# Kernel tuning notes

Measured on AMD Instinct MI355X. Metric: run time of the kernel, lower is better.

Reference implementation:

```python
import jax, jax.numpy as jnp
import numpy as np


def reference(x, edge_index, edge_attr, W, b):
    """PyG GCNConv: out = D^{-1/2} (A + I) D^{-1/2} X W + b.

    x: [N, Din] node features
    edge_index: [2, E] int (row=source, col=target)
    edge_attr: [E] edge weights
    W: [Din, Dout], b: [Dout]
    """
    N = x.shape[0]
    # add self-loops with weight 1 (PyG fill_value=1.0)
    loop = jnp.arange(N, dtype=edge_index.dtype)
    row = jnp.concatenate([edge_index[0], loop])
    col = jnp.concatenate([edge_index[1], loop])
    w = jnp.concatenate([edge_attr, jnp.ones((N,), dtype=edge_attr.dtype)])

    # symmetric normalization: norm_e = d[row]^-1/2 * w_e * d[col]^-1/2
    deg = jax.ops.segment_sum(w, col, num_segments=N)
    dis = jnp.where(deg > 0, jax.lax.rsqrt(jnp.where(deg > 0, deg, 1.0)), 0.0)
    norm = dis[row] * w * dis[col]

    # linear projection first (Din == Dout, cheaper either way), then
    # gather-scale-scatter aggregation at targets
    h = x @ W                                   # [N, Dout]
    msg = h[row] * norm[:, None]                # [E+N, Dout]
    out = jax.ops.segment_sum(msg, col, num_segments=N)  # [N, Dout]
    return out + b


def setup_inputs() -> dict:
    key = jax.random.key(0)
    k1, k2, k3, k4 = jax.random.split(key, 4)
    N, E, Din, Dout = 100000, 1600000, 128, 128
    x = jax.random.normal(k1, (N, Din), dtype=jnp.float32)
    edge_index = jax.random.randint(k2, (2, E), 0, N, dtype=jnp.int64)
    edge_attr = jax.random.uniform(k3, (E,), dtype=jnp.float32)
    # Glorot init like PyG Linear default
    W = jax.random.normal(k4, (Din, Dout), dtype=jnp.float32) * (1.0 / np.sqrt(Din))
    b = jnp.zeros((Dout,), dtype=jnp.float32)
    return {"x": x, "edge_index": edge_index, "edge_attr": edge_attr, "W": W, "b": b}
```

## Files before the change

### kernel.cpp

```cpp
#include <hip/hip_runtime.h>


#define ELEMS_PER_SCAN_BLOCK 4096
#define SCAN_SHIFT 12
#define CHUNK 2048
#define NCMAX 800

typedef __attribute__((ext_vector_type(8))) short short8;
typedef __attribute__((ext_vector_type(4))) float f32x4;

__device__ inline unsigned short f2bf(float f) {
    unsigned u = __float_as_uint(f);
    u += 0x7fffu + ((u >> 16) & 1u);
    return (unsigned short)(u >> 16);
}
__device__ inline float bf_lo(unsigned u) { return __uint_as_float(u << 16); }
__device__ inline float bf_hi(unsigned u) { return __uint_as_float(u & 0xffff0000u); }

__global__ __launch_bounds__(256) void k_hist(const int* __restrict__ col,
                                              const float* __restrict__ W,
                                              int* __restrict__ histg,
                                              unsigned short* __restrict__ Wtg,
                                              int E, int NC, int NBLK) {
    __shared__ int lh[1024];
    int t = threadIdx.x, blk = blockIdx.x;
    if (blk < 64) {
        int n = blk * 2 + (t >> 7);
        int k = t & 127;
        Wtg[n * 128 + k] = f2bf(W[k * 128 + n]);
    }
    for (int i = t; i < 1024; i += 256) lh[i] = 0;
    __syncthreads();
    int base = blk * CHUNK;
    #pragma unroll
    for (int i = 0; i < CHUNK / 256; ++i) {
        int e = base + i * 256 + t;
        if (e < E) atomicAdd(&lh[col[e] >> 7], 1);
    }
    __syncthreads();
    for (int b = t; b < NC; b += 256) histg[b * NBLK + blk] = lh[b];
}

__device__ inline int wave_incl_scan(int x, int lane) {
    #pragma unroll
    for (int d = 1; d < 64; d <<= 1) {
        int y = __shfl_up(x, d, 64);
        if (lane >= d) x += y;
    }
    return x;
}

__global__ void k_scan1(const int* __restrict__ in, int* __restrict__ out,
                        int* __restrict__ bsum, int M) {
    __shared__ int wsum[4];
    __shared__ int woff[4];
    int t = threadIdx.x, lane = t & 63, wid = t >> 6;
    int base = blockIdx.x * ELEMS_PER_SCAN_BLOCK + t * 16;
    int v[16];
    #pragma unroll
    for (int i = 0; i < 16; ++i) v[i] = (base + i < M) ? in[base + i] : 0;
    int run = 0;
    #pragma unroll
    for (int i = 0; i < 16; ++i) { int x = v[i]; v[i] = run; run += x; }
    int incl = wave_incl_scan(run, lane);
    int excl = incl - run;
    if (lane == 63) wsum[wid] = incl;
    __syncthreads();
    if (t == 0) {
        int r = 0;
        #pragma unroll
        for (int w = 0; w < 4; ++w) { int s = wsum[w]; woff[w] = r; r += s; }
        bsum[blockIdx.x] = r;
    }
    __syncthreads();
    int off = woff[wid] + excl;
    #pragma unroll
    for (int i = 0; i < 16; ++i)
        if (base + i < M) out[base + i] = v[i] + off;
}

__global__ void k_scan2(const int* __restrict__ bsum, int* __restrict__ boff, int NB) {
    __shared__ int wsum[4];
    __shared__ int woff[4];
    int t = threadIdx.x, lane = t & 63, wid = t >> 6;
    int x = (t < NB) ? bsum[t] : 0;
    int incl = wave_incl_scan(x, lane);
    int excl = incl - x;
    if (lane == 63) wsum[wid] = incl;
    __syncthreads();
    if (t == 0) {
        int r = 0;
        #pragma unroll
        for (int w = 0; w < 4; ++w) { int s = wsum[w]; woff[w] = r; r += s; }
    }
    __syncthreads();
    if (t < NB) boff[t] = woff[wid] + excl;
}

struct GSmem { short Xs[64][72]; short Ws[128][72]; };

__device__ __forceinline__ void gemm_body(GSmem& sm, const float* __restrict__ x,
                                          const unsigned short* __restrict__ Wtg,
                                          unsigned short* __restrict__ h,
                                          int row0, int N, int t) {
    int lane = t & 63, wid = t >> 6;
    int q = lane >> 4;
    int m = lane & 15;
    f32x4 acc[8];
    #pragma unroll
    for (int tde = 0; tde < 8; ++tde) acc[tde] = (f32x4){0.f, 0.f, 0.f, 0.f};

    #pragma unroll
    for (int kh = 0; kh < 2; ++kh) {
        {
            int r = t >> 2;
            int kf = (t & 3) * 16;
            int gr = row0 + r;
            const float4* src = (const float4*)(x + (size_t)gr * 128 + kh * 64 + kf);
            float4 a0 = make_float4(0.f, 0.f, 0.f, 0.f), a1 = a0, a2 = a0, a3 = a0;
            if (gr < N) { a0 = src[0]; a1 = src[1]; a2 = src[2]; a3 = src[3]; }
            short8 p0, p1;
            p0[0] = (short)f2bf(a0.x); p0[1] = (short)f2bf(a0.y);
            p0[2] = (short)f2bf(a0.z); p0[3] = (short)f2bf(a0.w);
            p0[4] = (short)f2bf(a1.x); p0[5] = (short)f2bf(a1.y);
            p0[6] = (short)f2bf(a1.z); p0[7] = (short)f2bf(a1.w);
            p1[0] = (short)f2bf(a2.x); p1[1] = (short)f2bf(a2.y);
            p1[2] = (short)f2bf(a2.z); p1[3] = (short)f2bf(a2.w);
            p1[4] = (short)f2bf(a3.x); p1[5] = (short)f2bf(a3.y);
            p1[6] = (short)f2bf(a3.z); p1[7] = (short)f2bf(a3.w);
            *(short8*)&sm.Xs[r][kf]     = p0;
            *(short8*)&sm.Xs[r][kf + 8] = p1;
        }
        {
            int n = t >> 1;
            int off = (t & 1) * 32;
            const short* wsrc = (const short*)Wtg + n * 128 + kh * 64 + off;
            #pragma unroll
            for (int i = 0; i < 4; ++i)
                *(short8*)&sm.Ws[n][off + 8 * i] = *(const short8*)(wsrc + 8 * i);
        }
        __syncthreads();
        #pragma unroll
        for (int kc = 0; kc < 64; kc += 32) {
            short8 af = *(const short8*)&sm.Xs[wid * 16 + m][kc + q * 8];
            #pragma unroll
            for (int tde = 0; tde < 8; ++tde) {
                short8 bf = *(const short8*)&sm.Ws[tde * 16 + m][kc + q * 8];
                acc[tde] = __builtin_amdgcn_mfma_f32_16x16x32_bf16(af, bf, acc[tde], 0, 0, 0);
            }
        }
        __syncthreads();
    }
    #pragma unroll
    for (int r = 0; r < 4; ++r) {
        int grow = row0 + wid * 16 + q * 4 + r;
        if (grow < N) {
            #pragma unroll
            for (int tde = 0; tde < 8; ++tde)
                h[(size_t)grow * 128 + tde * 16 + m] = f2bf(acc[tde][r]);
        }
    }
}

__global__ __launch_bounds__(256) void k_pg(const int* __restrict__ row,
                                            const int* __restrict__ col,
                                            const float* __restrict__ wgt,
                                            const int* __restrict__ histg,
                                            const int* __restrict__ boff,
                                            int2* __restrict__ srw,
                                            const float* __restrict__ x,
                                            const unsigned short* __restrict__ Wtg,
                                            unsigned short* __restrict__ h,
                                            int E, int N, int NC, int NBLK) {
    __shared__ union {
        struct { int lcnt[NCMAX]; int gadj[NCMAX]; int2 stage[CHUNK]; int sdst[CHUNK];
                 int wsum[4]; int woff[4]; } p;
        GSmem g;
    } sm;
    int t = threadIdx.x;
    if ((int)blockIdx.x >= NBLK) {
        gemm_body(sm.g, x, Wtg, h, ((int)blockIdx.x - NBLK) * 64, N, t);
        return;
    }
    int blk = blockIdx.x;
    int lane = t & 63, wid = t >> 6;
    int base = blk * CHUNK;
    int nE = min(CHUNK, E - base);
    for (int b = t; b < NCMAX; b += 256) sm.p.lcnt[b] = 0;
    __syncthreads();
    #pragma unroll
    for (int i = 0; i < CHUNK / 256; ++i) {
        int e = base + i * 256 + t;
        if (e < E) atomicAdd(&sm.p.lcnt[col[e] >> 7], 1);
    }
    __syncthreads();
    int c4[4];
    int sum = 0;
    #pragma unroll
    for (int i = 0; i < 4; ++i) {
        int idx = t * 4 + i;
        int v = (idx < NCMAX) ? sm.p.lcnt[idx] : 0;
        c4[i] = sum; sum += v;
    }
    int incl = wave_incl_scan(sum, lane);
    int excl = incl - sum;
    if (lane == 63) sm.p.wsum[wid] = incl;
    __syncthreads();
    if (t == 0) {
        int r = 0;
        #pragma unroll
        for (int w = 0; w < 4; ++w) { int s = sm.p.wsum[w]; sm.p.woff[w] = r; r += s; }
    }
    __syncthreads();
    int tb = sm.p.woff[wid] + excl;
    __syncthreads();
    #pragma unroll
    for (int i = 0; i < 4; ++i) {
        int idx = t * 4 + i;
        if (idx < NCMAX) {
            int b0 = tb + c4[i];
            int gb = 0;
            if (idx < NC) {
                int g = idx * NBLK + blk;
                gb = histg[g] + boff[g >> SCAN_SHIFT];
            }
            sm.p.gadj[idx] = gb - b0;
            sm.p.lcnt[idx] = b0;
        }
    }
    __syncthreads();
    #pragma unroll
    for (int i = 0; i < CHUNK / 256; ++i) {
        int e = base + i * 256 + t;
        if (e < E) {
            int c = col[e];
            int slot = atomicAdd(&sm.p.lcnt[c >> 7], 1);
            sm.p.stage[slot] = make_int2(((c & 127) << 17) | row[e], __float_as_int(wgt[e]));
            sm.p.sdst[slot] = sm.p.gadj[c >> 7] + slot;
        }
    }
    __syncthreads();
    for (int s_ = t; s_ < nE; s_ += 256) {
        srw[sm.p.sdst[s_]] = sm.p.stage[s_];
    }
}

__global__ __launch_bounds__(256) void k_fine(const int* __restrict__ histg,
                                              const int* __restrict__ boff,
                                              const int2* __restrict__ srw,
                                              int* __restrict__ rowptr,
                                              float* __restrict__ dis,
                                              int2* __restrict__ spack,
                                              int E, int N, int NC, int NBLK) {
    __shared__ struct { int2 sbuf[3072]; int cnt128[128]; float degf[128];
                        int cur128[128]; int wtot[2]; } sf;
    int t = threadIdx.x, b = blockIdx.x;
    int nb = b << 7;
    int g0 = b * NBLK;
    int start = histg[g0] + boff[g0 >> SCAN_SHIFT];
    int end;
    if (b == NC - 1) end = E;
    else {
        int g1 = (b + 1) * NBLK;
        end = histg[g1] + boff[g1 >> SCAN_SHIFT];
    }
    int cnt = end - start;
    int NL = min(cnt, 3072);
    if (t < 128) { sf.cnt128[t] = 0; sf.degf[t] = 1.0f; }
    __syncthreads();
    for (int j = t; j < cnt; j += 256) {
        int2 s = srw[start + j];
        if (j < NL) sf.sbuf[j] = s;
        int c = s.x >> 17;
        atomicAdd(&sf.cnt128[c], 1);
        atomicAdd(&sf.degf[c], __int_as_float(s.y));
    }
    __syncthreads();
    int v = 0, incl = 0;
    if (t < 128) {
        v = sf.cnt128[t];
        incl = wave_incl_scan(v, t & 63);
        if ((t & 63) == 63) sf.wtot[t >> 6] = incl;
    }
    __syncthreads();
    if (t < 128) {
        int excl = incl - v + ((t >= 64) ? sf.wtot[0] : 0);
        int p = start + excl;
        sf.cur128[t] = p;
        int n = nb + t;
        if (n < N) {
            rowptr[n] = p;
            dis[n] = rsqrtf(sf.degf[t]);
        }
    }
    if (t == 0 && b == NC - 1) rowptr[N] = E;
    __syncthreads();
    for (int j = t; j < cnt; j += 256) {
        int2 s = (j < NL) ? sf.sbuf[j] : srw[start + j];
        int c = s.x >> 17;
        int pos = atomicAdd(&sf.cur128[c], 1);
        spack[pos] = make_int2(s.x & 0x1FFFF, s.y);
    }
}

__global__ __launch_bounds__(256) void k_gather(const unsigned int* __restrict__ hb,
                                                const float* __restrict__ dis,
                                                const int* __restrict__ rowptr,
                                                const long* __restrict__ spackl,
                                                const float* __restrict__ bias,
                                                float* __restrict__ out, int N) {
    int gid = blockIdx.x * blockDim.x + threadIdx.x;
    int node = gid >> 6;
    int lane = gid & 63;
    if (node >= N) return;
    node = __builtin_amdgcn_readfirstlane(node);

    float dn = dis[node];
    unsigned u = hb[(size_t)node * 64 + lane];
    float2 acc;
    acc.x = dn * bf_lo(u);
    acc.y = dn * bf_hi(u);

    int jb = rowptr[node], je = rowptr[node + 1];
    int j = jb;
    long q0, q1, q2, q3, q4, q5, q6, q7;
    if (j + 8 <= je) {
        q0 = __builtin_nontemporal_load(spackl + j);
        q1 = __builtin_nontemporal_load(spackl + j + 1);
        q2 = __builtin_nontemporal_load(spackl + j + 2);
        q3 = __builtin_nontemporal_load(spackl + j + 3);
        q4 = __builtin_nontemporal_load(spackl + j + 4);
        q5 = __builtin_nontemporal_load(spackl + j + 5);
        q6 = __builtin_nontemporal_load(spackl + j + 6);
        q7 = __builtin_nontemporal_load(spackl + j + 7);
    }
    for (; j + 8 <= je; j += 8) {
        int r0 = __builtin_amdgcn_readfirstlane((int)q0);
        int r1 = __builtin_amdgcn_readfirstlane((int)q1);
        int r2 = __builtin_amdgcn_readfirstlane((int)q2);
        int r3 = __builtin_amdgcn_readfirstlane((int)q3);
        int r4 = __builtin_amdgcn_readfirstlane((int)q4);
        int r5 = __builtin_amdgcn_readfirstlane((int)q5);
        int r6 = __builtin_amdgcn_readfirstlane((int)q6);
        int r7 = __builtin_amdgcn_readfirstlane((int)q7);
        unsigned u0 = hb[(size_t)r0 * 64 + lane];
        unsigned u1 = hb[(size_t)r1 * 64 + lane];
        unsigned u2 = hb[(size_t)r2 * 64 + lane];
        unsigned u3 = hb[(size_t)r3 * 64 + lane];
        unsigned u4 = hb[(size_t)r4 * 64 + lane];
        unsigned u5 = hb[(size_t)r5 * 64 + lane];
        unsigned u6 = hb[(size_t)r6 * 64 + lane];
        unsigned u7 = hb[(size_t)r7 * 64 + lane];
        int jn = (j + 16 <= je) ? j + 8 : j;
        long n0 = __builtin_nontemporal_load(spackl + jn);
        long n1 = __builtin_nontemporal_load(spackl + jn + 1);
        long n2 = __builtin_nontemporal_load(spackl + jn + 2);
        long n3 = __builtin_nontemporal_load(spackl + jn + 3);
        long n4 = __builtin_nontemporal_load(spackl + jn + 4);
        long n5 = __builtin_nontemporal_load(spackl + jn + 5);
        long n6 = __builtin_nontemporal_load(spackl + jn + 6);
        long n7 = __builtin_nontemporal_load(spackl + jn + 7);
        float a0 = dis[r0] * __uint_as_float((unsigned)((unsigned long)q0 >> 32));
        float a1 = dis[r1] * __uint_as_float((unsigned)((unsigned long)q1 >> 32));
        float a2 = dis[r2] * __uint_as_float((unsigned)((unsigned long)q2 >> 32));
        float a3 = dis[r3] * __uint_as_float((unsigned)((unsigned long)q3 >> 32));
        float a4 = dis[r4] * __uint_as_float((unsigned)((unsigned long)q4 >> 32));
        float a5 = dis[r5] * __uint_as_float((unsigned)((unsigned long)q5 >> 32));
        float a6 = dis[r6] * __uint_as_float((unsigned)((unsigned long)q6 >> 32));
        float a7 = dis[r7] * __uint_as_float((unsigned)((unsigned long)q7 >> 32));
        acc.x = fmaf(a0, bf_lo(u0), acc.x); acc.y = fmaf(a0, bf_hi(u0), acc.y);
        acc.x = fmaf(a1, bf_lo(u1), acc.x); acc.y = fmaf(a1, bf_hi(u1), acc.y);
        acc.x = fmaf(a2, bf_lo(u2), acc.x); acc.y = fmaf(a2, bf_hi(u2), acc.y);
        acc.x = fmaf(a3, bf_lo(u3), acc.x); acc.y = fmaf(a3, bf_hi(u3), acc.y);
        acc.x = fmaf(a4, bf_lo(u4), acc.x); acc.y = fmaf(a4, bf_hi(u4), acc.y);
        acc.x = fmaf(a5, bf_lo(u5), acc.x); acc.y = fmaf(a5, bf_hi(u5), acc.y);
        acc.x = fmaf(a6, bf_lo(u6), acc.x); acc.y = fmaf(a6, bf_hi(u6), acc.y);
        acc.x = fmaf(a7, bf_lo(u7), acc.x); acc.y = fmaf(a7, bf_hi(u7), acc.y);
        q0 = n0; q1 = n1; q2 = n2; q3 = n3; q4 = n4; q5 = n5; q6 = n6; q7 = n7;
    }
    for (; j < je; ++j) {
        long q = __builtin_nontemporal_load(spackl + j);
        int r = __builtin_amdgcn_readfirstlane((int)q);
        unsigned uu = hb[(size_t)r * 64 + lane];
        float a = dis[r] * __uint_as_float((unsigned)((unsigned long)q >> 32));
        acc.x = fmaf(a, bf_lo(uu), acc.x);
        acc.y = fmaf(a, bf_hi(uu), acc.y);
    }

    int c0 = lane * 2;
    float2 bv = *(const float2*)(bias + c0);
    float2 o;
    o.x = bv.x + dn * acc.x;
    o.y = bv.y + dn * acc.y;
    union { float2 f; double d; } cvt;
    cvt.f = o;
    __builtin_nontemporal_store(cvt.d, (double*)(out + (size_t)node * 128 + c0));
}

extern "C" void kernel_launch(void* const* d_in, const int* in_sizes, int n_in,
                              void* d_out, int out_size, void* d_ws, size_t ws_size,
                              hipStream_t stream) {
    const float* x     = (const float*)d_in[0];
    const int*   eidx  = (const int*)d_in[1];
    const float* eattr = (const float*)d_in[2];
    const float* W     = (const float*)d_in[3];
    const float* bias  = (const float*)d_in[4];
    int N = in_sizes[0] / 128;
    int E = in_sizes[2];
    const int* row = eidx;
    const int* col = eidx + E;

    int NC = (N + 127) >> 7;
    int NBLK = (E + CHUNK - 1) / CHUNK;

    char* p = (char*)d_ws;
    auto carve = [&](size_t bytes) {
        char* q = p;
        p += (bytes + 255) & ~(size_t)255;
        return q;
    };
    unsigned short* h   = (unsigned short*)carve((size_t)N * 128 * sizeof(unsigned short));
    unsigned short* Wtg = (unsigned short*)carve(128 * 128 * sizeof(unsigned short));
    float* dis    = (float*)carve((size_t)N * sizeof(float));
    int*   rowptr = (int*)carve((size_t)(N + 1) * sizeof(int));
    int*   histg  = (int*)carve((size_t)NC * NBLK * sizeof(int));
    int2*  srw    = (int2*)carve((size_t)E * sizeof(int2));
    int2*  spack  = (int2*)carve((size_t)E * sizeof(int2));
    int*   bsum   = (int*)carve(256 * sizeof(int));
    int*   boff   = (int*)carve(256 * sizeof(int));

    int M = NC * NBLK;
    int NBs = (M + ELEMS_PER_SCAN_BLOCK - 1) / ELEMS_PER_SCAN_BLOCK;
    int GB = (N + 63) / 64;

    k_hist<<<NBLK, 256, 0, stream>>>(col, W, histg, Wtg, E, NC, NBLK);
    k_scan1<<<NBs, 256, 0, stream>>>(histg, histg, bsum, M);
    k_scan2<<<1, 256, 0, stream>>>(bsum, boff, NBs);
    k_pg<<<NBLK + GB, 256, 0, stream>>>(row, col, eattr, histg, boff, srw,
                                        x, Wtg, h, E, N, NC, NBLK);
    k_fine<<<NC, 256, 0, stream>>>(histg, boff, srw, rowptr, dis, spack, E, N, NC, NBLK);
    {
        size_t threads = (size_t)N * 64;
        int blocks = (int)((threads + 255) / 256);
        k_gather<<<blocks, 256, 0, stream>>>((const unsigned int*)h, dis, rowptr,
                                             (const long*)spack, bias, (float*)d_out, N);
    }
}
```

Before: 248.5 us.

## Spread GEMM tiles across scan, pg and fine kernels to fill idle CUs

The X·W projection, which previously ran entirely as extra blocks of the partition kernel, is split into four slices. The slices are appended as extra blocks to the scan1, scan2, pg and fine kernels, so the tiny latency-bound scan kernels and the fine bucketing kernel share the GPU with GEMM work. The W transpose moves into its own small kernel launched first, which adds one launch. Adding the GEMM shared-memory union to the scan kernels raises their LDS footprint, which may reduce occupancy for the scan blocks.

```diff
diff --git a/kernel.cpp b/kernel.cpp
--- a/kernel.cpp
+++ b/kernel.cpp
@@ -17,18 +17,17 @@
 __device__ inline float bf_lo(unsigned u) { return __uint_as_float(u << 16); }
 __device__ inline float bf_hi(unsigned u) { return __uint_as_float(u & 0xffff0000u); }
 
+__global__ void k_wprep(const float* __restrict__ W, unsigned short* __restrict__ Wtg) {
+    int n = blockIdx.x;
+    int k = threadIdx.x;
+    Wtg[n * 128 + k] = f2bf(W[k * 128 + n]);
+}
+
 __global__ __launch_bounds__(256) void k_hist(const int* __restrict__ col,
-                                              const float* __restrict__ W,
                                               int* __restrict__ histg,
-                                              unsigned short* __restrict__ Wtg,
                                               int E, int NC, int NBLK) {
     __shared__ int lh[1024];
     int t = threadIdx.x, blk = blockIdx.x;
-    if (blk < 64) {
-        int n = blk * 2 + (t >> 7);
-        int k = t & 127;
-        Wtg[n * 128 + k] = f2bf(W[k * 128 + n]);
-    }
     for (int i = t; i < 1024; i += 256) lh[i] = 0;
     __syncthreads();
     int base = blk * CHUNK;
@@ -48,53 +47,6 @@
         if (lane >= d) x += y;
     }
     return x;
-}
-
-__global__ void k_scan1(const int* __restrict__ in, int* __restrict__ out,
-                        int* __restrict__ bsum, int M) {
-    __shared__ int wsum[4];
-    __shared__ int woff[4];
-    int t = threadIdx.x, lane = t & 63, wid = t >> 6;
-    int base = blockIdx.x * ELEMS_PER_SCAN_BLOCK + t * 16;
-    int v[16];
-    #pragma unroll
-    for (int i = 0; i < 16; ++i) v[i] = (base + i < M) ? in[base + i] : 0;
-    int run = 0;
-    #pragma unroll
-    for (int i = 0; i < 16; ++i) { int x = v[i]; v[i] = run; run += x; }
-    int incl = wave_incl_scan(run, lane);
-    int excl = incl - run;
-    if (lane == 63) wsum[wid] = incl;
-    __syncthreads();
-    if (t == 0) {
-        int r = 0;
-        #pragma unroll
-        for (int w = 0; w < 4; ++w) { int s = wsum[w]; woff[w] = r; r += s; }
-        bsum[blockIdx.x] = r;
-    }
-    __syncthreads();
-    int off = woff[wid] + excl;
-    #pragma unroll
-    for (int i = 0; i < 16; ++i)
-        if (base + i < M) out[base + i] = v[i] + off;
-}
-
-__global__ void k_scan2(const int* __restrict__ bsum, int* __restrict__ boff, int NB) {
-    __shared__ int wsum[4];
-    __shared__ int woff[4];
-    int t = threadIdx.x, lane = t & 63, wid = t >> 6;
-    int x = (t < NB) ? bsum[t] : 0;
-    int incl = wave_incl_scan(x, lane);
-    int excl = incl - x;
-    if (lane == 63) wsum[wid] = incl;
-    __syncthreads();
-    if (t == 0) {
-        int r = 0;
-        #pragma unroll
-        for (int w = 0; w < 4; ++w) { int s = wsum[w]; woff[w] = r; r += s; }
-    }
-    __syncthreads();
-    if (t < NB) boff[t] = woff[wid] + excl;
 }
 
 struct GSmem { short Xs[64][72]; short Ws[128][72]; };
@@ -162,6 +114,71 @@
     }
 }
 
+__global__ __launch_bounds__(256) void k_scan1(const int* __restrict__ in,
+                                               int* __restrict__ out,
+                                               int* __restrict__ bsum, int M,
+                                               const float* __restrict__ x,
+                                               const unsigned short* __restrict__ Wtg,
+                                               unsigned short* __restrict__ h,
+                                               int N, int NSC, int gbase) {
+    __shared__ union { struct { int wsum[4]; int woff[4]; } s; GSmem g; } sm;
+    int t = threadIdx.x;
+    if ((int)blockIdx.x >= NSC) {
+        gemm_body(sm.g, x, Wtg, h, (gbase + (int)blockIdx.x - NSC) * 64, N, t);
+        return;
+    }
+    int lane = t & 63, wid = t >> 6;
+    int base = blockIdx.x * ELEMS_PER_SCAN_BLOCK + t * 16;
+    int v[16];
+    #pragma unroll
+    for (int i = 0; i < 16; ++i) v[i] = (base + i < M) ? in[base + i] : 0;
+    int run = 0;
+    #pragma unroll
+    for (int i = 0; i < 16; ++i) { int xk = v[i]; v[i] = run; run += xk; }
+    int incl = wave_incl_scan(run, lane);
+    int excl = incl - run;
+    if (lane == 63) sm.s.wsum[wid] = incl;
+    __syncthreads();
+    if (t == 0) {
+        int r = 0;
+        #pragma unroll
+        for (int w = 0; w < 4; ++w) { int s = sm.s.wsum[w]; sm.s.woff[w] = r; r += s; }
+        bsum[blockIdx.x] = r;
+    }
+    __syncthreads();
+    int off = sm.s.woff[wid] + excl;
+    #pragma unroll
+    for (int i = 0; i < 16; ++i)
+        if (base + i < M) out[base + i] = v[i] + off;
+}
+
+__global__ __launch_bounds__(256) void k_scan2(const int* __restrict__ bsum,
+                                               int* __restrict__ boff, int NB,
+                                               const float* __restrict__ x,
+                                               const unsigned short* __restrict__ Wtg,
+                                               unsigned short* __restrict__ h,
+                                               int N, int gbase) {
+    __shared__ union { struct { int wsum[4]; int woff[4]; } s; GSmem g; } sm;
+    int t = threadIdx.x;
+    if ((int)blockIdx.x >= 1) {
+        gemm_body(sm.g, x, Wtg, h, (gbase + (int)blockIdx.x - 1) * 64, N, t);
+        return;
+    }
+    int lane = t & 63, wid = t >> 6;
+    int xk = (t < NB) ? bsum[t] : 0;
+    int incl = wave_incl_scan(xk, lane);
+    int excl = incl - xk;
+    if (lane == 63) sm.s.wsum[wid] = incl;
+    __syncthreads();
+    if (t == 0) {
+        int r = 0;
+        #pragma unroll
+        for (int w = 0; w < 4; ++w) { int s = sm.s.wsum[w]; sm.s.woff[w] = r; r += s; }
+    }
+    __syncthreads();
+    if (t < NB) boff[t] = sm.s.woff[wid] + excl;
+}
+
 __global__ __launch_bounds__(256) void k_pg(const int* __restrict__ row,
                                             const int* __restrict__ col,
                                             const float* __restrict__ wgt,
@@ -171,7 +188,7 @@
                                             const float* __restrict__ x,
                                             const unsigned short* __restrict__ Wtg,
                                             unsigned short* __restrict__ h,
-                                            int E, int N, int NC, int NBLK) {
+                                            int E, int N, int NC, int NBLK, int gbase) {
     __shared__ union {
         struct { int lcnt[NCMAX]; int gadj[NCMAX]; int2 stage[CHUNK]; int sdst[CHUNK];
                  int wsum[4]; int woff[4]; } p;
@@ -179,7 +196,7 @@
     } sm;
     int t = threadIdx.x;
     if ((int)blockIdx.x >= NBLK) {
-        gemm_body(sm.g, x, Wtg, h, ((int)blockIdx.x - NBLK) * 64, N, t);
+        gemm_body(sm.g, x, Wtg, h, (gbase + (int)blockIdx.x - NBLK) * 64, N, t);
         return;
     }
     int blk = blockIdx.x;
@@ -251,10 +268,21 @@
                                               int* __restrict__ rowptr,
                                               float* __restrict__ dis,
                                               int2* __restrict__ spack,
-                                              int E, int N, int NC, int NBLK) {
-    __shared__ struct { int2 sbuf[3072]; int cnt128[128]; float degf[128];
-                        int cur128[128]; int wtot[2]; } sf;
-    int t = threadIdx.x, b = blockIdx.x;
+                                              const float* __restrict__ x,
+                                              const unsigned short* __restrict__ Wtg,
+                                              unsigned short* __restrict__ h,
+                                              int E, int N, int NC, int NBLK, int gbase) {
+    __shared__ union {
+        struct { int2 sbuf[3072]; int cnt128[128]; float degf[128];
+                 int cur128[128]; int wtot[2]; } f;
+        GSmem g;
+    } sm;
+    int t = threadIdx.x;
+    if ((int)blockIdx.x >= NC) {
+        gemm_body(sm.g, x, Wtg, h, (gbase + (int)blockIdx.x - NC) * 64, N, t);
+        return;
+    }
+    int b = blockIdx.x;
     int nb = b << 7;
     int g0 = b * NBLK;
     int start = histg[g0] + boff[g0 >> SCAN_SHIFT];
@@ -266,39 +294,39 @@
     }
     int cnt = end - start;
     int NL = min(cnt, 3072);
-    if (t < 128) { sf.cnt128[t] = 0; sf.degf[t] = 1.0f; }
+    if (t < 128) { sm.f.cnt128[t] = 0; sm.f.degf[t] = 1.0f; }
     __syncthreads();
     for (int j = t; j < cnt; j += 256) {
         int2 s = srw[start + j];
-        if (j < NL) sf.sbuf[j] = s;
+        if (j < NL) sm.f.sbuf[j] = s;
         int c = s.x >> 17;
-        atomicAdd(&sf.cnt128[c], 1);
-        atomicAdd(&sf.degf[c], __int_as_float(s.y));
+        atomicAdd(&sm.f.cnt128[c], 1);
+        atomicAdd(&sm.f.degf[c], __int_as_float(s.y));
     }
     __syncthreads();
     int v = 0, incl = 0;
     if (t < 128) {
-        v = sf.cnt128[t];
+        v = sm.f.cnt128[t];
         incl = wave_incl_scan(v, t & 63);
-        if ((t & 63) == 63) sf.wtot[t >> 6] = incl;
+        if ((t & 63) == 63) sm.f.wtot[t >> 6] = incl;
     }
     __syncthreads();
     if (t < 128) {
-        int excl = incl - v + ((t >= 64) ? sf.wtot[0] : 0);
+        int excl = incl - v + ((t >= 64) ? sm.f.wtot[0] : 0);
         int p = start + excl;
-        sf.cur128[t] = p;
+        sm.f.cur128[t] = p;
         int n = nb + t;
         if (n < N) {
             rowptr[n] = p;
-            dis[n] = rsqrtf(sf.degf[t]);
+            dis[n] = rsqrtf(sm.f.degf[t]);
         }
     }
     if (t == 0 && b == NC - 1) rowptr[N] = E;
     __syncthreads();
     for (int j = t; j < cnt; j += 256) {
-        int2 s = (j < NL) ? sf.sbuf[j] : srw[start + j];
+        int2 s = (j < NL) ? sm.f.sbuf[j] : srw[start + j];
         int c = s.x >> 17;
-        int pos = atomicAdd(&sf.cur128[c], 1);
+        int pos = atomicAdd(&sm.f.cur128[c], 1);
         spack[pos] = make_int2(s.x & 0x1FFFF, s.y);
     }
 }
@@ -432,13 +460,21 @@
     int M = NC * NBLK;
     int NBs = (M + ELEMS_PER_SCAN_BLOCK - 1) / ELEMS_PER_SCAN_BLOCK;
     int GB = (N + 63) / 64;
-
-    k_hist<<<NBLK, 256, 0, stream>>>(col, W, histg, Wtg, E, NC, NBLK);
-    k_scan1<<<NBs, 256, 0, stream>>>(histg, histg, bsum, M);
-    k_scan2<<<1, 256, 0, stream>>>(bsum, boff, NBs);
-    k_pg<<<NBLK + GB, 256, 0, stream>>>(row, col, eattr, histg, boff, srw,
-                                        x, Wtg, h, E, N, NC, NBLK);
-    k_fine<<<NC, 256, 0, stream>>>(histg, boff, srw, rowptr, dis, spack, E, N, NC, NBLK);
+    int GBa = GB / 4;
+    int GBb = GB / 4;
+    int GBc = GB / 4;
+    int GBd = GB - GBa - GBb - GBc;
+
+    k_wprep<<<128, 128, 0, stream>>>(W, Wtg);
+    k_hist<<<NBLK, 256, 0, stream>>>(col, histg, E, NC, NBLK);
+    k_scan1<<<NBs + GBa, 256, 0, stream>>>(histg, histg, bsum, M,
+                                           x, Wtg, h, N, NBs, 0);
+    k_scan2<<<1 + GBb, 256, 0, stream>>>(bsum, boff, NBs,
+                                         x, Wtg, h, N, GBa);
+    k_pg<<<NBLK + GBc, 256, 0, stream>>>(row, col, eattr, histg, boff, srw,
+                                         x, Wtg, h, E, N, NC, NBLK, GBa + GBb);
+    k_fine<<<NC + GBd, 256, 0, stream>>>(histg, boff, srw, rowptr, dis, spack,
+                                         x, Wtg, h, E, N, NC, NBLK, GBa + GBb + GBc);
     {
         size_t threads = (size_t)N * 64;
         int blocks = (int)((threads + 255) / 256);
```

Result: slower. 258.5 us (+4.0%).

## Split GEMM blocks across histogram and partition kernels, simplify gather prefetch

Applied to the files above, without the earlier changes.

The dense X·W projection blocks are now split in half. One half rides along in the histogram kernel and the other half stays in the partition kernel, so both passes have extra compute to overlap with their memory-bound edge work. The W transpose-to-bf16 moves into its own small kernel launched first, because the histogram kernel's GEMM blocks now depend on it. The gather kernel drops its software-pipelined prefetch of the next 8 packed edges and loads them at the top of each iteration instead, which lowers register pressure but gives up some load overlap. The extra launch and the loss of prefetch could offset part of the benefit.

```diff
diff --git a/kernel.cpp b/kernel.cpp
--- a/kernel.cpp
+++ b/kernel.cpp
@@ -17,28 +17,10 @@
 __device__ inline float bf_lo(unsigned u) { return __uint_as_float(u << 16); }
 __device__ inline float bf_hi(unsigned u) { return __uint_as_float(u & 0xffff0000u); }
 
-__global__ __launch_bounds__(256) void k_hist(const int* __restrict__ col,
-                                              const float* __restrict__ W,
-                                              int* __restrict__ histg,
-                                              unsigned short* __restrict__ Wtg,
-                                              int E, int NC, int NBLK) {
-    __shared__ int lh[1024];
-    int t = threadIdx.x, blk = blockIdx.x;
-    if (blk < 64) {
-        int n = blk * 2 + (t >> 7);
-        int k = t & 127;
-        Wtg[n * 128 + k] = f2bf(W[k * 128 + n]);
-    }
-    for (int i = t; i < 1024; i += 256) lh[i] = 0;
-    __syncthreads();
-    int base = blk * CHUNK;
-    #pragma unroll
-    for (int i = 0; i < CHUNK / 256; ++i) {
-        int e = base + i * 256 + t;
-        if (e < E) atomicAdd(&lh[col[e] >> 7], 1);
-    }
-    __syncthreads();
-    for (int b = t; b < NC; b += 256) histg[b * NBLK + blk] = lh[b];
+__global__ void k_wprep(const float* __restrict__ W, unsigned short* __restrict__ Wtg) {
+    int n = blockIdx.x;
+    int k = threadIdx.x;
+    Wtg[n * 128 + k] = f2bf(W[k * 128 + n]);
 }
 
 __device__ inline int wave_incl_scan(int x, int lane) {
@@ -48,53 +30,6 @@
         if (lane >= d) x += y;
     }
     return x;
-}
-
-__global__ void k_scan1(const int* __restrict__ in, int* __restrict__ out,
-                        int* __restrict__ bsum, int M) {
-    __shared__ int wsum[4];
-    __shared__ int woff[4];
-    int t = threadIdx.x, lane = t & 63, wid = t >> 6;
-    int base = blockIdx.x * ELEMS_PER_SCAN_BLOCK + t * 16;
-    int v[16];
-    #pragma unroll
-    for (int i = 0; i < 16; ++i) v[i] = (base + i < M) ? in[base + i] : 0;
-    int run = 0;
-    #pragma unroll
-    for (int i = 0; i < 16; ++i) { int x = v[i]; v[i] = run; run += x; }
-    int incl = wave_incl_scan(run, lane);
-    int excl = incl - run;
-    if (lane == 63) wsum[wid] = incl;
-    __syncthreads();
-    if (t == 0) {
-        int r = 0;
-        #pragma unroll
-        for (int w = 0; w < 4; ++w) { int s = wsum[w]; woff[w] = r; r += s; }
-        bsum[blockIdx.x] = r;
-    }
-    __syncthreads();
-    int off = woff[wid] + excl;
-    #pragma unroll
-    for (int i = 0; i < 16; ++i)
-        if (base + i < M) out[base + i] = v[i] + off;
-}
-
-__global__ void k_scan2(const int* __restrict__ bsum, int* __restrict__ boff, int NB) {
-    __shared__ int wsum[4];
-    __shared__ int woff[4];
-    int t = threadIdx.x, lane = t & 63, wid = t >> 6;
-    int x = (t < NB) ? bsum[t] : 0;
-    int incl = wave_incl_scan(x, lane);
-    int excl = incl - x;
-    if (lane == 63) wsum[wid] = incl;
-    __syncthreads();
-    if (t == 0) {
-        int r = 0;
-        #pragma unroll
-        for (int w = 0; w < 4; ++w) { int s = wsum[w]; woff[w] = r; r += s; }
-    }
-    __syncthreads();
-    if (t < NB) boff[t] = woff[wid] + excl;
 }
 
 struct GSmem { short Xs[64][72]; short Ws[128][72]; };
@@ -162,6 +97,78 @@
     }
 }
 
+__global__ __launch_bounds__(256) void k_hist(const int* __restrict__ col,
+                                              int* __restrict__ histg,
+                                              const float* __restrict__ x,
+                                              const unsigned short* __restrict__ Wtg,
+                                              unsigned short* __restrict__ h,
+                                              int E, int N, int NC, int NBLK, int gbase) {
+    __shared__ union { int lh[1024]; GSmem g; } sm;
+    int t = threadIdx.x;
+    if ((int)blockIdx.x >= NBLK) {
+        gemm_body(sm.g, x, Wtg, h, (gbase + (int)blockIdx.x - NBLK) * 64, N, t);
+        return;
+    }
+    int blk = blockIdx.x;
+    for (int i = t; i < 1024; i += 256) sm.lh[i] = 0;
+    __syncthreads();
+    int base = blk * CHUNK;
+    #pragma unroll
+    for (int i = 0; i < CHUNK / 256; ++i) {
+        int e = base + i * 256 + t;
+        if (e < E) atomicAdd(&sm.lh[col[e] >> 7], 1);
+    }
+    __syncthreads();
+    for (int b = t; b < NC; b += 256) histg[b * NBLK + blk] = sm.lh[b];
+}
+
+__global__ void k_scan1(const int* __restrict__ in, int* __restrict__ out,
+                        int* __restrict__ bsum, int M) {
+    __shared__ int wsum[4];
+    __shared__ int woff[4];
+    int t = threadIdx.x, lane = t & 63, wid = t >> 6;
+    int base = blockIdx.x * ELEMS_PER_SCAN_BLOCK + t * 16;
+    int v[16];
+    #pragma unroll
+    for (int i = 0; i < 16; ++i) v[i] = (base + i < M) ? in[base + i] : 0;
+    int run = 0;
+    #pragma unroll
+    for (int i = 0; i < 16; ++i) { int x = v[i]; v[i] = run; run += x; }
+    int incl = wave_incl_scan(run, lane);
+    int excl = incl - run;
+    if (lane == 63) wsum[wid] = incl;
+    __syncthreads();
+    if (t == 0) {
+        int r = 0;
+        #pragma unroll
+        for (int w = 0; w < 4; ++w) { int s = wsum[w]; woff[w] = r; r += s; }
+        bsum[blockIdx.x] = r;
+    }
+    __syncthreads();
+    int off = woff[wid] + excl;
+    #pragma unroll
+    for (int i = 0; i < 16; ++i)
+        if (base + i < M) out[base + i] = v[i] + off;
+}
+
+__global__ void k_scan2(const int* __restrict__ bsum, int* __restrict__ boff, int NB) {
+    __shared__ int wsum[4];
+    __shared__ int woff[4];
+    int t = threadIdx.x, lane = t & 63, wid = t >> 6;
+    int x = (t < NB) ? bsum[t] : 0;
+    int incl = wave_incl_scan(x, lane);
+    int excl = incl - x;
+    if (lane == 63) wsum[wid] = incl;
+    __syncthreads();
+    if (t == 0) {
+        int r = 0;
+        #pragma unroll
+        for (int w = 0; w < 4; ++w) { int s = wsum[w]; woff[w] = r; r += s; }
+    }
+    __syncthreads();
+    if (t < NB) boff[t] = woff[wid] + excl;
+}
+
 __global__ __launch_bounds__(256) void k_pg(const int* __restrict__ row,
                                             const int* __restrict__ col,
                                             const float* __restrict__ wgt,
@@ -171,7 +178,7 @@
                                             const float* __restrict__ x,
                                             const unsigned short* __restrict__ Wtg,
                                             unsigned short* __restrict__ h,
-                                            int E, int N, int NC, int NBLK) {
+                                            int E, int N, int NC, int NBLK, int gbase) {
     __shared__ union {
         struct { int lcnt[NCMAX]; int gadj[NCMAX]; int2 stage[CHUNK]; int sdst[CHUNK];
                  int wsum[4]; int woff[4]; } p;
@@ -179,7 +186,7 @@
     } sm;
     int t = threadIdx.x;
     if ((int)blockIdx.x >= NBLK) {
-        gemm_body(sm.g, x, Wtg, h, ((int)blockIdx.x - NBLK) * 64, N, t);
+        gemm_body(sm.g, x, Wtg, h, (gbase + (int)blockIdx.x - NBLK) * 64, N, t);
         return;
     }
     int blk = blockIdx.x;
@@ -323,18 +330,15 @@
 
     int jb = rowptr[node], je = rowptr[node + 1];
     int j = jb;
-    long q0, q1, q2, q3, q4, q5, q6, q7;
-    if (j + 8 <= je) {
-        q0 = __builtin_nontemporal_load(spackl + j);
-        q1 = __builtin_nontemporal_load(spackl + j + 1);
-        q2 = __builtin_nontemporal_load(spackl + j + 2);
-        q3 = __builtin_nontemporal_load(spackl + j + 3);
-        q4 = __builtin_nontemporal_load(spackl + j + 4);
-        q5 = __builtin_nontemporal_load(spackl + j + 5);
-        q6 = __builtin_nontemporal_load(spackl + j + 6);
-        q7 = __builtin_nontemporal_load(spackl + j + 7);
-    }
     for (; j + 8 <= je; j += 8) {
+        long q0 = __builtin_nontemporal_load(spackl + j);
+        long q1 = __builtin_nontemporal_load(spackl + j + 1);
+        long q2 = __builtin_nontemporal_load(spackl + j + 2);
+        long q3 = __builtin_nontemporal_load(spackl + j + 3);
+        long q4 = __builtin_nontemporal_load(spackl + j + 4);
+        long q5 = __builtin_nontemporal_load(spackl + j + 5);
+        long q6 = __builtin_nontemporal_load(spackl + j + 6);
+        long q7 = __builtin_nontemporal_load(spackl + j + 7);
         int r0 = __builtin_amdgcn_readfirstlane((int)q0);
         int r1 = __builtin_amdgcn_readfirstlane((int)q1);
         int r2 = __builtin_amdgcn_readfirstlane((int)q2);
@@ -351,15 +355,6 @@
         unsigned u5 = hb[(size_t)r5 * 64 + lane];
         unsigned u6 = hb[(size_t)r6 * 64 + lane];
         unsigned u7 = hb[(size_t)r7 * 64 + lane];
-        int jn = (j + 16 <= je) ? j + 8 : j;
-        long n0 = __builtin_nontemporal_load(spackl + jn);
-        long n1 = __builtin_nontemporal_load(spackl + jn + 1);
-        long n2 = __builtin_nontemporal_load(spackl + jn + 2);
-        long n3 = __builtin_nontemporal_load(spackl + jn + 3);
-        long n4 = __builtin_nontemporal_load(spackl + jn + 4);
-        long n5 = __builtin_nontemporal_load(spackl + jn + 5);
-        long n6 = __builtin_nontemporal_load(spackl + jn + 6);
-        long n7 = __builtin_nontemporal_load(spackl + jn + 7);
         float a0 = dis[r0] * __uint_as_float((unsigned)((unsigned long)q0 >> 32));
         float a1 = dis[r1] * __uint_as_float((unsigned)((unsigned long)q1 >> 32));
         float a2 = dis[r2] * __uint_as_float((unsigned)((unsigned long)q2 >> 32));
@@ -376,7 +371,6 @@
         acc.x = fmaf(a5, bf_lo(u5), acc.x); acc.y = fmaf(a5, bf_hi(u5), acc.y);
         acc.x = fmaf(a6, bf_lo(u6), acc.x); acc.y = fmaf(a6, bf_hi(u6), acc.y);
         acc.x = fmaf(a7, bf_lo(u7), acc.x); acc.y = fmaf(a7, bf_hi(u7), acc.y);
-        q0 = n0; q1 = n1; q2 = n2; q3 = n3; q4 = n4; q5 = n5; q6 = n6; q7 = n7;
     }
     for (; j < je; ++j) {
         long q = __builtin_nontemporal_load(spackl + j);
@@ -431,13 +425,17 @@
 
     int M = NC * NBLK;
     int NBs = (M + ELEMS_PER_SCAN_BLOCK - 1) / ELEMS_PER_SCAN_BLOCK;
-    int GB = (N + 63) / 64;
-
-    k_hist<<<NBLK, 256, 0, stream>>>(col, W, histg, Wtg, E, NC, NBLK);
+    int GB  = (N + 63) / 64;
+    int GB1 = GB / 2;
+    int GB2 = GB - GB1;
+
+    k_wprep<<<128, 128, 0, stream>>>(W, Wtg);
+    k_hist<<<NBLK + GB1, 256, 0, stream>>>(col, histg, x, Wtg, h,
+                                           E, N, NC, NBLK, 0);
     k_scan1<<<NBs, 256, 0, stream>>>(histg, histg, bsum, M);
     k_scan2<<<1, 256, 0, stream>>>(bsum, boff, NBs);
-    k_pg<<<NBLK + GB, 256, 0, stream>>>(row, col, eattr, histg, boff, srw,
-                                        x, Wtg, h, E, N, NC, NBLK);
+    k_pg<<<NBLK + GB2, 256, 0, stream>>>(row, col, eattr, histg, boff, srw,
+                                         x, Wtg, h, E, N, NC, NBLK, GB1);
     k_fine<<<NC, 256, 0, stream>>>(histg, boff, srw, rowptr, dis, spack, E, N, NC, NBLK);
     {
         size_t threads = (size_t)N * 64;
```

Measured after the change: 255.2 us. +2.7%, slower.

## Fold source-degree scaling into GEMM output and drop dis gather in aggregation

Applied to the files above, without the earlier changes.

Splits the fused placement+GEMM kernel back into separate kernels and runs the GEMM after k_fine, so that h is pre-scaled by dis[row] at write time. This removes the per-edge random dis[r] load in the gather kernel. The gather loop's software prefetch of the next edge batch is also removed. In exchange the GEMM no longer overlaps with edge placement, and the bf16 rounding now applies to the scaled values.

```diff
diff --git a/kernel.cpp b/kernel.cpp
--- a/kernel.cpp
+++ b/kernel.cpp
@@ -97,13 +97,144 @@
     if (t < NB) boff[t] = woff[wid] + excl;
 }
 
-struct GSmem { short Xs[64][72]; short Ws[128][72]; };
-
-__device__ __forceinline__ void gemm_body(GSmem& sm, const float* __restrict__ x,
-                                          const unsigned short* __restrict__ Wtg,
-                                          unsigned short* __restrict__ h,
-                                          int row0, int N, int t) {
+__global__ __launch_bounds__(256) void k_place(const int* __restrict__ row,
+                                               const int* __restrict__ col,
+                                               const float* __restrict__ wgt,
+                                               const int* __restrict__ histg,
+                                               const int* __restrict__ boff,
+                                               int2* __restrict__ srw,
+                                               int E, int NC, int NBLK) {
+    __shared__ struct { int lcnt[NCMAX]; int gadj[NCMAX]; int2 stage[CHUNK];
+                        int sdst[CHUNK]; int wsum[4]; int woff[4]; } sp;
+    int t = threadIdx.x, blk = blockIdx.x;
     int lane = t & 63, wid = t >> 6;
+    int base = blk * CHUNK;
+    int nE = min(CHUNK, E - base);
+    for (int b = t; b < NCMAX; b += 256) sp.lcnt[b] = 0;
+    __syncthreads();
+    #pragma unroll
+    for (int i = 0; i < CHUNK / 256; ++i) {
+        int e = base + i * 256 + t;
+        if (e < E) atomicAdd(&sp.lcnt[col[e] >> 7], 1);
+    }
+    __syncthreads();
+    int c4[4];
+    int sum = 0;
+    #pragma unroll
+    for (int i = 0; i < 4; ++i) {
+        int idx = t * 4 + i;
+        int v = (idx < NCMAX) ? sp.lcnt[idx] : 0;
+        c4[i] = sum; sum += v;
+    }
+    int incl = wave_incl_scan(sum, lane);
+    int excl = incl - sum;
+    if (lane == 63) sp.wsum[wid] = incl;
+    __syncthreads();
+    if (t == 0) {
+        int r = 0;
+        #pragma unroll
+        for (int w = 0; w < 4; ++w) { int s = sp.wsum[w]; sp.woff[w] = r; r += s; }
+    }
+    __syncthreads();
+    int tb = sp.woff[wid] + excl;
+    __syncthreads();
+    #pragma unroll
+    for (int i = 0; i < 4; ++i) {
+        int idx = t * 4 + i;
+        if (idx < NCMAX) {
+            int b0 = tb + c4[i];
+            int gb = 0;
+            if (idx < NC) {
+                int g = idx * NBLK + blk;
+                gb = histg[g] + boff[g >> SCAN_SHIFT];
+            }
+            sp.gadj[idx] = gb - b0;
+            sp.lcnt[idx] = b0;
+        }
+    }
+    __syncthreads();
+    #pragma unroll
+    for (int i = 0; i < CHUNK / 256; ++i) {
+        int e = base + i * 256 + t;
+        if (e < E) {
+            int c = col[e];
+            int slot = atomicAdd(&sp.lcnt[c >> 7], 1);
+            sp.stage[slot] = make_int2(((c & 127) << 17) | row[e], __float_as_int(wgt[e]));
+            sp.sdst[slot] = sp.gadj[c >> 7] + slot;
+        }
+    }
+    __syncthreads();
+    for (int s_ = t; s_ < nE; s_ += 256) {
+        srw[sp.sdst[s_]] = sp.stage[s_];
+    }
+}
+
+__global__ __launch_bounds__(256) void k_fine(const int* __restrict__ histg,
+                                              const int* __restrict__ boff,
+                                              const int2* __restrict__ srw,
+                                              int* __restrict__ rowptr,
+                                              float* __restrict__ dis,
+                                              int2* __restrict__ spack,
+                                              int E, int N, int NC, int NBLK) {
+    __shared__ struct { int2 sbuf[3072]; int cnt128[128]; float degf[128];
+                        int cur128[128]; int wtot[2]; } sf;
+    int t = threadIdx.x, b = blockIdx.x;
+    int nb = b << 7;
+    int g0 = b * NBLK;
+    int start = histg[g0] + boff[g0 >> SCAN_SHIFT];
+    int end;
+    if (b == NC - 1) end = E;
+    else {
+        int g1 = (b + 1) * NBLK;
+        end = histg[g1] + boff[g1 >> SCAN_SHIFT];
+    }
+    int cnt = end - start;
+    int NL = min(cnt, 3072);
+    if (t < 128) { sf.cnt128[t] = 0; sf.degf[t] = 1.0f; }
+    __syncthreads();
+    for (int j = t; j < cnt; j += 256) {
+        int2 s = srw[start + j];
+        if (j < NL) sf.sbuf[j] = s;
+        int c = s.x >> 17;
+        atomicAdd(&sf.cnt128[c], 1);
+        atomicAdd(&sf.degf[c], __int_as_float(s.y));
+    }
+    __syncthreads();
+    int v = 0, incl = 0;
+    if (t < 128) {
+        v = sf.cnt128[t];
+        incl = wave_incl_scan(v, t & 63);
+        if ((t & 63) == 63) sf.wtot[t >> 6] = incl;
+    }
+    __syncthreads();
+    if (t < 128) {
+        int excl = incl - v + ((t >= 64) ? sf.wtot[0] : 0);
+        int p = start + excl;
+        sf.cur128[t] = p;
+        int n = nb + t;
+        if (n < N) {
+            rowptr[n] = p;
+            dis[n] = rsqrtf(sf.degf[t]);
+        }
+    }
+    if (t == 0 && b == NC - 1) rowptr[N] = E;
+    __syncthreads();
+    for (int j = t; j < cnt; j += 256) {
+        int2 s = (j < NL) ? sf.sbuf[j] : srw[start + j];
+        int c = s.x >> 17;
+        int pos = atomicAdd(&sf.cur128[c], 1);
+        spack[pos] = make_int2(s.x & 0x1FFFF, s.y);
+    }
+}
+
+__global__ __launch_bounds__(256) void k_gemm(const float* __restrict__ x,
+                                              const unsigned short* __restrict__ Wtg,
+                                              const float* __restrict__ dis,
+                                              unsigned short* __restrict__ h, int N) {
+    __shared__ struct { short Xs[64][72]; short Ws[128][72]; } sm;
+    int t = threadIdx.x;
+    int lane = t & 63, wid = t >> 6;
+    int row0 = blockIdx.x * 64;
     int q = lane >> 4;
     int m = lane & 15;
     f32x4 acc[8];
@@ -155,151 +286,11 @@
     for (int r = 0; r < 4; ++r) {
         int grow = row0 + wid * 16 + q * 4 + r;
         if (grow < N) {
+            float dn = dis[grow];
             #pragma unroll
             for (int tde = 0; tde < 8; ++tde)
-                h[(size_t)grow * 128 + tde * 16 + m] = f2bf(acc[tde][r]);
-        }
-    }
-}
-
-__global__ __launch_bounds__(256) void k_pg(const int* __restrict__ row,
-                                            const int* __restrict__ col,
-                                            const float* __restrict__ wgt,
-                                            const int* __restrict__ histg,
-                                            const int* __restrict__ boff,
-                                            int2* __restrict__ srw,
-                                            const float* __restrict__ x,
-                                            const unsigned short* __restrict__ Wtg,
-                                            unsigned short* __restrict__ h,
-                                            int E, int N, int NC, int NBLK) {
-    __shared__ union {
-        struct { int lcnt[NCMAX]; int gadj[NCMAX]; int2 stage[CHUNK]; int sdst[CHUNK];
-                 int wsum[4]; int woff[4]; } p;
-        GSmem g;
-    } sm;
-    int t = threadIdx.x;
-    if ((int)blockIdx.x >= NBLK) {
-        gemm_body(sm.g, x, Wtg, h, ((int)blockIdx.x - NBLK) * 64, N, t);
-        return;
-    }
-    int blk = blockIdx.x;
-    int lane = t & 63, wid = t >> 6;
-    int base = blk * CHUNK;
-    int nE = min(CHUNK, E - base);
-    for (int b = t; b < NCMAX; b += 256) sm.p.lcnt[b] = 0;
-    __syncthreads();
-    #pragma unroll
-    for (int i = 0; i < CHUNK / 256; ++i) {
-        int e = base + i * 256 + t;
-        if (e < E) atomicAdd(&sm.p.lcnt[col[e] >> 7], 1);
-    }
-    __syncthreads();
-    int c4[4];
-    int sum = 0;
-    #pragma unroll
-    for (int i = 0; i < 4; ++i) {
-        int idx = t * 4 + i;
-        int v = (idx < NCMAX) ? sm.p.lcnt[idx] : 0;
-        c4[i] = sum; sum += v;
-    }
-    int incl = wave_incl_scan(sum, lane);
-    int excl = incl - sum;
-    if (lane == 63) sm.p.wsum[wid] = incl;
-    __syncthreads();
-    if (t == 0) {
-        int r = 0;
-        #pragma unroll
-        for (int w = 0; w < 4; ++w) { int s = sm.p.wsum[w]; sm.p.woff[w] = r; r += s; }
-    }
-    __syncthreads();
-    int tb = sm.p.woff[wid] + excl;
-    __syncthreads();
-    #pragma unroll
-    for (int i = 0; i < 4; ++i) {
-        int idx = t * 4 + i;
-        if (idx < NCMAX) {
-            int b0 = tb + c4[i];
-            int gb = 0;
-            if (idx < NC) {
-                int g = idx * NBLK + blk;
-                gb = histg[g] + boff[g >> SCAN_SHIFT];
-            }
-            sm.p.gadj[idx] = gb - b0;
-            sm.p.lcnt[idx] = b0;
-        }
-    }
-    __syncthreads();
-    #pragma unroll
-    for (int i = 0; i < CHUNK / 256; ++i) {
-        int e = base + i * 256 + t;
-        if (e < E) {
-            int c = col[e];
-            int slot = atomicAdd(&sm.p.lcnt[c >> 7], 1);
-            sm.p.stage[slot] = make_int2(((c & 127) << 17) | row[e], __float_as_int(wgt[e]));
-            sm.p.sdst[slot] = sm.p.gadj[c >> 7] + slot;
-        }
-    }
-    __syncthreads();
-    for (int s_ = t; s_ < nE; s_ += 256) {
-        srw[sm.p.sdst[s_]] = sm.p.stage[s_];
-    }
-}
-
-__global__ __launch_bounds__(256) void k_fine(const int* __restrict__ histg,
-                                              const int* __restrict__ boff,
-                                              const int2* __restrict__ srw,
-                                              int* __restrict__ rowptr,
-                                              float* __restrict__ dis,
-                                              int2* __restrict__ spack,
-                                              int E, int N, int NC, int NBLK) {
-    __shared__ struct { int2 sbuf[3072]; int cnt128[128]; float degf[128];
-                        int cur128[128]; int wtot[2]; } sf;
-    int t = threadIdx.x, b = blockIdx.x;
-    int nb = b << 7;
-    int g0 = b * NBLK;
-    int start = histg[g0] + boff[g0 >> SCAN_SHIFT];
-    int end;
-    if (b == NC - 1) end = E;
-    else {
-        int g1 = (b + 1) * NBLK;
-        end = histg[g1] + boff[g1 >> SCAN_SHIFT];
-    }
-    int cnt = end - start;
-    int NL = min(cnt, 3072);
-    if (t < 128) { sf.cnt128[t] = 0; sf.degf[t] = 1.0f; }
-    __syncthreads();
-    for (int j = t; j < cnt; j += 256) {
-        int2 s = srw[start + j];
-        if (j < NL) sf.sbuf[j] = s;
-        int c = s.x >> 17;
-        atomicAdd(&sf.cnt128[c], 1);
-        atomicAdd(&sf.degf[c], __int_as_float(s.y));
-    }
-    __syncthreads();
-    int v = 0, incl = 0;
-    if (t < 128) {
-        v = sf.cnt128[t];
-        incl = wave_incl_scan(v, t & 63);
-        if ((t & 63) == 63) sf.wtot[t >> 6] = incl;
-    }
-    __syncthreads();
-    if (t < 128) {
-        int excl = incl - v + ((t >= 64) ? sf.wtot[0] : 0);
-        int p = start + excl;
-        sf.cur128[t] = p;
-        int n = nb + t;
-        if (n < N) {
-            rowptr[n] = p;
-            dis[n] = rsqrtf(sf.degf[t]);
-        }
-    }
-    if (t == 0 && b == NC - 1) rowptr[N] = E;
-    __syncthreads();
-    for (int j = t; j < cnt; j += 256) {
-        int2 s = (j < NL) ? sf.sbuf[j] : srw[start + j];
-        int c = s.x >> 17;
-        int pos = atomicAdd(&sf.cur128[c], 1);
-        spack[pos] = make_int2(s.x & 0x1FFFF, s.y);
+                h[(size_t)grow * 128 + tde * 16 + m] = f2bf(dn * acc[tde][r]);
+        }
     }
 }
 
@@ -318,23 +309,20 @@
     float dn = dis[node];
     unsigned u = hb[(size_t)node * 64 + lane];
     float2 acc;
-    acc.x = dn * bf_lo(u);
-    acc.y = dn * bf_hi(u);
+    acc.x = bf_lo(u);
+    acc.y = bf_hi(u);
 
     int jb = rowptr[node], je = rowptr[node + 1];
     int j = jb;
-    long q0, q1, q2, q3, q4, q5, q6, q7;
-    if (j + 8 <= je) {
-        q0 = __builtin_nontemporal_load(spackl + j);
-        q1 = __builtin_nontemporal_load(spackl + j + 1);
-        q2 = __builtin_nontemporal_load(spackl + j + 2);
-        q3 = __builtin_nontemporal_load(spackl + j + 3);
-        q4 = __builtin_nontemporal_load(spackl + j + 4);
-        q5 = __builtin_nontemporal_load(spackl + j + 5);
-        q6 = __builtin_nontemporal_load(spackl + j + 6);
-        q7 = __builtin_nontemporal_load(spackl + j + 7);
-    }
     for (; j + 8 <= je; j += 8) {
+        long q0 = __builtin_nontemporal_load(spackl + j);
+        long q1 = __builtin_nontemporal_load(spackl + j + 1);
+        long q2 = __builtin_nontemporal_load(spackl + j + 2);
+        long q3 = __builtin_nontemporal_load(spackl + j + 3);
+        long q4 = __builtin_nontemporal_load(spackl + j + 4);
+        long q5 = __builtin_nontemporal_load(spackl + j + 5);
+        long q6 = __builtin_nontemporal_load(spackl + j + 6);
+        long q7 = __builtin_nontemporal_load(spackl + j + 7);
         int r0 = __builtin_amdgcn_readfirstlane((int)q0);
         int r1 = __builtin_amdgcn_readfirstlane((int)q1);
         int r2 = __builtin_amdgcn_readfirstlane((int)q2);
@@ -351,23 +339,14 @@
         unsigned u5 = hb[(size_t)r5 * 64 + lane];
         unsigned u6 = hb[(size_t)r6 * 64 + lane];
         unsigned u7 = hb[(size_t)r7 * 64 + lane];
-        int jn = (j + 16 <= je) ? j + 8 : j;
-        long n0 = __builtin_nontemporal_load(spackl + jn);
-        long n1 = __builtin_nontemporal_load(spackl + jn + 1);
-        long n2 = __builtin_nontemporal_load(spackl + jn + 2);
-        long n3 = __builtin_nontemporal_load(spackl + jn + 3);
-        long n4 = __builtin_nontemporal_load(spackl + jn + 4);
-        long n5 = __builtin_nontemporal_load(spackl + jn + 5);
-        long n6 = __builtin_nontemporal_load(spackl + jn + 6);
-        long n7 = __builtin_nontemporal_load(spackl + jn + 7);
-        float a0 = dis[r0] * __uint_as_float((unsigned)((unsigned long)q0 >> 32));
-        float a1 = dis[r1] * __uint_as_float((unsigned)((unsigned long)q1 >> 32));
-        float a2 = dis[r2] * __uint_as_float((unsigned)((unsigned long)q2 >> 32));
-        float a3 = dis[r3] * __uint_as_float((unsigned)((unsigned long)q3 >> 32));
-        float a4 = dis[r4] * __uint_as_float((unsigned)((unsigned long)q4 >> 32));
-        float a5 = dis[r5] * __uint_as_float((unsigned)((unsigned long)q5 >> 32));
-        float a6 = dis[r6] * __uint_as_float((unsigned)((unsigned long)q6 >> 32));
-        float a7 = dis[r7] * __uint_as_float((unsigned)((unsigned long)q7 >> 32));
+        float a0 = __uint_as_float((unsigned)((unsigned long)q0 >> 32));
+        float a1 = __uint_as_float((unsigned)((unsigned long)q1 >> 32));
+        float a2 = __uint_as_float((unsigned)((unsigned long)q2 >> 32));
+        float a3 = __uint_as_float((unsigned)((unsigned long)q3 >> 32));
+        float a4 = __uint_as_float((unsigned)((unsigned long)q4 >> 32));
+        float a5 = __uint_as_float((unsigned)((unsigned long)q5 >> 32));
+        float a6 = __uint_as_float((unsigned)((unsigned long)q6 >> 32));
+        float a7 = __uint_as_float((unsigned)((unsigned long)q7 >> 32));
         acc.x = fmaf(a0, bf_lo(u0), acc.x); acc.y = fmaf(a0, bf_hi(u0), acc.y);
         acc.x = fmaf(a1, bf_lo(u1), acc.x); acc.y = fmaf(a1, bf_hi(u1), acc.y);
         acc.x = fmaf(a2, bf_lo(u2), acc.x); acc.y = fmaf(a2, bf_hi(u2), acc.y);
@@ -376,13 +355,12 @@
         acc.x = fmaf(a5, bf_lo(u5), acc.x); acc.y = fmaf(a5, bf_hi(u5), acc.y);
         acc.x = fmaf(a6, bf_lo(u6), acc.x); acc.y = fmaf(a6, bf_hi(u6), acc.y);
         acc.x = fmaf(a7, bf_lo(u7), acc.x); acc.y = fmaf(a7, bf_hi(u7), acc.y);
-        q0 = n0; q1 = n1; q2 = n2; q3 = n3; q4 = n4; q5 = n5; q6 = n6; q7 = n7;
     }
     for (; j < je; ++j) {
         long q = __builtin_nontemporal_load(spackl + j);
         int r = __builtin_amdgcn_readfirstlane((int)q);
         unsigned uu = hb[(size_t)r * 64 + lane];
-        float a = dis[r] * __uint_as_float((unsigned)((unsigned long)q >> 32));
+        float a = __uint_as_float((unsigned)((unsigned long)q >> 32));
         acc.x = fmaf(a, bf_lo(uu), acc.x);
         acc.y = fmaf(a, bf_hi(uu), acc.y);
     }
@@ -436,9 +414,9 @@
     k_hist<<<NBLK, 256, 0, stream>>>(col, W, histg, Wtg, E, NC, NBLK);
     k_scan1<<<NBs, 256, 0, stream>>>(histg, histg, bsum, M);
     k_scan2<<<1, 256, 0, stream>>>(bsum, boff, NBs);
-    k_pg<<<NBLK + GB, 256, 0, stream>>>(row, col, eattr, histg, boff, srw,
-                                        x, Wtg, h, E, N, NC, NBLK);
+    k_place<<<NBLK, 256, 0, stream>>>(row, col, eattr, histg, boff, srw, E, NC, NBLK);
     k_fine<<<NC, 256, 0, stream>>>(histg, boff, srw, rowptr, dis, spack, E, N, NC, NBLK);
+    k_gemm<<<GB, 256, 0, stream>>>(x, Wtg, dis, h, N);
     {
         size_t threads = (size_t)N * 64;
         int blocks = (int)((threads + 255) / 256);
```

Result: no change. 248.9 us (+0.2%).
